# Kernel tuning notes

Hardware: AMD Instinct MI355X
Metric: run time of the kernel (lower is better)

## Reference

```python
import jax, jax.numpy as jnp
import numpy as np

N_EMBEDDING = 32
HEAD_SIZE = 64
B, T = 8, 4096


def setup_inputs() -> dict:
    key = jax.random.key(0)
    kx, kk, kq, kv = jax.random.split(key, 4)
    x = jax.random.normal(kx, (B, T, N_EMBEDDING), dtype=jnp.float32)
    Wk = jax.random.normal(kk, (N_EMBEDDING, HEAD_SIZE), dtype=jnp.float32) * 0.05
    Wq = jax.random.normal(kq, (N_EMBEDDING, HEAD_SIZE), dtype=jnp.float32) * 0.05
    Wv = jax.random.normal(kv, (N_EMBEDDING, HEAD_SIZE), dtype=jnp.float32) * 0.05
    return {"x": x, "Wk": Wk, "Wq": Wq, "Wv": Wv}


def reference(x, Wk, Wq, Wv):
    # x: [B, T, C]; projections (no bias)
    k = jnp.einsum("btc,cd->btd", x, Wk)  # [B,T,D]
    q = jnp.einsum("btc,cd->btd", x, Wq)
    v = jnp.einsum("btc,cd->btd", x, Wv)
    # raw scores (NOTE: original module applies no 1/sqrt(D) scaling)
    wei = jnp.einsum("bqd,bkd->bqk", q, k)  # [B,T,T]
    t = x.shape[1]
    causal = jnp.tril(jnp.ones((t, t), dtype=bool))
    wei = jnp.where(causal[None, :, :], wei, -jnp.inf)
    wei = jax.nn.softmax(wei, axis=-1)
    out = jnp.einsum("bqk,bkd->bqd", wei, v)  # [B,T,D]
    return out
```

## Files before the change

kernel.cpp:

```cpp
#include <hip/hip_runtime.h>
#include <hip/hip_bf16.h>

constexpr int Bc = 8;
constexpr int Tt = 4096;
constexpr int Dd = 64;

typedef __attribute__((ext_vector_type(8))) short short8;
typedef __attribute__((ext_vector_type(4))) float floatx4;
typedef uint4   __attribute__((may_alias)) uint4_a;
typedef short8  __attribute__((may_alias)) short8_a;
typedef ushort4 __attribute__((may_alias)) ushort4_a;
typedef float4  __attribute__((may_alias)) float4_a;

#define MFMA16(A, B, C) __builtin_amdgcn_mfma_f32_16x16x32_bf16(A, B, C, 0, 0, 0)
constexpr float LOG2E = 1.4426950408889634f;

__device__ __forceinline__ unsigned rnd16(float x) {
    unsigned u; __builtin_memcpy(&u, &x, 4); return u + 0x8000u;
}
__device__ __forceinline__ unsigned pk_bf2(float lo, float hi) {
    return __builtin_amdgcn_perm(rnd16(hi), rnd16(lo), 0x07060302);
}
__device__ __forceinline__ ushort4 pack4(floatx4 d) {
    union { unsigned u[2]; ushort4 v; } r;
    r.u[0] = pk_bf2(d[0], d[1]);
    r.u[1] = pk_bf2(d[2], d[3]);
    return r.v;
}
__device__ __forceinline__ short8 cvt8(float4 a, float4 b) {
    union { unsigned u[4]; short8 s; } r;
    r.u[0] = pk_bf2(a.x, a.y);
    r.u[1] = pk_bf2(a.z, a.w);
    r.u[2] = pk_bf2(b.x, b.y);
    r.u[3] = pk_bf2(b.z, b.w);
    return r.s;
}

__global__ __launch_bounds__(1024, 4) void attn_kernel(
    const float* __restrict__ x,
    const float* __restrict__ Wk, const float* __restrict__ Wq,
    const float* __restrict__ Wv,
    float* __restrict__ out)
{
    __shared__ uint4 sStage[4096];
    __shared__ uint4 sP[2048];

    int b  = blockIdx.x & 7;
    int pr = blockIdx.x >> 3;
    int tid  = threadIdx.x;
    int wave = tid >> 6, lane = tid & 63;
    int group = wave >> 2, gw = wave & 3;
    int ln15 = lane & 15, quad = lane >> 4;
    int tid_g = tid & 255;
    size_t bT = (size_t)b * Tt;

    short8 wv_f[4];
    #pragma unroll
    for (int t = 0; t < 4; ++t) {
        int col = 16*t + ln15;
        union { unsigned u[4]; short8 s; } rv;
        #pragma unroll
        for (int jj = 0; jj < 4; ++jj) {
            const float* v0 = Wv + (quad*8 + 2*jj) * 64 + col;
            rv.u[jj] = pk_bf2(v0[0], v0[64]);
        }
        wv_f[t] = rv.s;
    }

    if (wave == 0) {
        floatx4 gC[2][2];
        #pragma unroll
        for (int mt = 0; mt < 2; ++mt)
            #pragma unroll
            for (int nt = 0; nt < 2; ++nt) gC[mt][nt] = (floatx4){0.f,0.f,0.f,0.f};
        #pragma unroll
        for (int kt = 0; kt < 2; ++kt) {
            short8 aG[2], bG[2];
            #pragma unroll
            for (int mt = 0; mt < 2; ++mt) {
                const float* qp = Wq + (ln15 + 16*mt)*64 + 32*kt + quad*8;
                float4 a = ((const float4_a*)qp)[0], bb = ((const float4_a*)qp)[1];
                a.x*=LOG2E; a.y*=LOG2E; a.z*=LOG2E; a.w*=LOG2E;
                bb.x*=LOG2E; bb.y*=LOG2E; bb.z*=LOG2E; bb.w*=LOG2E;
                aG[mt] = cvt8(a, bb);
                const float* kp = Wk + (ln15 + 16*mt)*64 + 32*kt + quad*8;
                bG[mt] = cvt8(((const float4_a*)kp)[0], ((const float4_a*)kp)[1]);
            }
            #pragma unroll
            for (int mt = 0; mt < 2; ++mt)
                #pragma unroll
                for (int nt = 0; nt < 2; ++nt)
                    gC[mt][nt] = MFMA16(aG[mt], bG[nt], gC[mt][nt]);
        }
        unsigned short* sGh = (unsigned short*)sP;
        #pragma unroll
        for (int mt = 0; mt < 2; ++mt)
            #pragma unroll
            for (int nt = 0; nt < 2; ++nt)
                *(ushort4_a*)(sGh + (16*nt + ln15)*32 + 16*mt + quad*4)
                    = pack4(gC[mt][nt]);
    }
    __syncthreads();
    short8 gt[2];
    #pragma unroll
    for (int mt = 0; mt < 2; ++mt) {
        union { uint4 u; short8 s; } g;
        g.u = sP[(16*mt + ln15)*4 + quad];
        gt[mt] = g.s;
    }
    __syncthreads();

    const int gBase = group * 1024;
    const int cT = tid_g & 31, kgT = tid_g >> 5;
    unsigned short* sYh = (unsigned short*)sP;

    #pragma unroll
    for (int phase = 0; phase < 2; ++phase) {
        const int qtP = phase ? pr : 63 - pr;
        const int q0 = qtP * 64;
        const int qrow = q0 + gw*16 + ln15;

        float4 pX0, pX1; float pT[8];
        if (group <= qtP) {
            const float* xp = x + (bT + group*64 + 16*gw + ln15)*32 + quad*8;
            pX0 = ((const float4_a*)xp)[0];
            pX1 = ((const float4_a*)xp)[1];
            const float* tp = x + (bT + group*64 + kgT*8)*32 + cT;
            #pragma unroll
            for (int j = 0; j < 8; ++j) pT[j] = tp[j*32];
        }

        if (wave < 8) {
            int qs = wave & 3, mt = wave >> 2;
            const float* xp = x + (bT + q0 + qs*16 + ln15)*32 + quad*8;
            short8 xq = cvt8(((const float4_a*)xp)[0], ((const float4_a*)xp)[1]);
            floatx4 d = (floatx4){0.f,0.f,0.f,0.f};
            d = MFMA16(gt[mt], xq, d);
            *(ushort4_a*)(sYh + (qs*16 + ln15)*32 + 16*mt + quad*4) = pack4(d);
        }
        __syncthreads();
        short8 bq;
        {
            union { uint4 u; short8 s; } t0;
            t0.u = sP[(gw*16 + ln15)*4 + quad];
            bq = t0.s;
        }

        floatx4 z4[2];
        z4[0] = (floatx4){0.f,0.f,0.f,0.f};
        z4[1] = (floatx4){0.f,0.f,0.f,0.f};
        float l_lane = 0.f;

        const int nIter = (qtP + 4) >> 2;

        for (int it = 0; it < nIter; ++it) {
            int kt = 4*it + group;
            bool active = (kt <= qtP);
            const int stB = gBase + (it & 1) * 512;
            if (active) {
                union { short8 s; uint4 u; } xu;
                xu.s = cvt8(pX0, pX1);
                sStage[stB + (16*gw + ln15)*4 + quad] = xu.u;
                uint4 xt;
                xt.x = pk_bf2(pT[0], pT[1]); xt.y = pk_bf2(pT[2], pT[3]);
                xt.z = pk_bf2(pT[4], pT[5]); xt.w = pk_bf2(pT[6], pT[7]);
                sStage[stB + 256 + cT*8 + (kgT ^ (cT & 7))] = xt;
            }
            __syncthreads();
            int ktn = kt + 4;
            if (ktn <= qtP) {
                const float* xp = x +
                    (bT + ktn*64 + 16*gw + ln15)*32 + quad*8;
                pX0 = ((const float4_a*)xp)[0];
                pX1 = ((const float4_a*)xp)[1];
                const float* tp = x + (bT + ktn*64 + kgT*8)*32 + cT;
                #pragma unroll
                for (int j = 0; j < 8; ++j) pT[j] = tp[j*32];
            }
            if (!active) continue;
            int k0 = kt * 64;

            floatx4 s4[4];
            #pragma unroll
            for (int t = 0; t < 4; ++t) {
                union { uint4 u; short8 s; } a;
                a.u = sStage[stB + (16*t + ln15)*4 + quad];
                floatx4 c = (floatx4){0.f,0.f,0.f,0.f};
                c = MFMA16(a.s, bq, c);
                s4[t] = c;
            }

            unsigned long long* sP64 = (unsigned long long*)sP;
            const int pb = wave*256 + ln15*16;
            const int xk = ln15 & 14;
            if (kt == qtP) {
                #pragma unroll
                for (int t = 0; t < 4; ++t) {
                    int keyb = k0 + 16*t + quad*4;
                    float p[4];
                    #pragma unroll
                    for (int r = 0; r < 4; ++r) {
                        p[r] = (keyb + r <= qrow) ? __builtin_amdgcn_exp2f(s4[t][r]) : 0.f;
                        l_lane += p[r];
                    }
                    unsigned long long pk =
                        ((unsigned long long)pk_bf2(p[2], p[3]) << 32) | pk_bf2(p[0], p[1]);
                    sP64[pb + ((4*t + quad) ^ xk)] = pk;
                }
            } else {
                #pragma unroll
                for (int t = 0; t < 4; ++t) {
                    float p[4];
                    #pragma unroll
                    for (int r = 0; r < 4; ++r) {
                        p[r] = __builtin_amdgcn_exp2f(s4[t][r]);
                        l_lane += p[r];
                    }
                    unsigned long long pk =
                        ((unsigned long long)pk_bf2(p[2], p[3]) << 32) | pk_bf2(p[0], p[1]);
                    sP64[pb + ((4*t + quad) ^ xk)] = pk;
                }
            }

            int h = (ln15 >> 1) & 7;
            union { uint4 u; short8 s; } p0, p1;
            p0.u = sP[wave*128 + ln15*8 + (quad ^ h)];
            p1.u = sP[wave*128 + ln15*8 + ((quad + 4) ^ h)];
            #pragma unroll
            for (int mt = 0; mt < 2; ++mt) {
                int row = 16*mt + ln15;
                union { uint4 u; short8 s; } a0, a1;
                a0.u = sStage[stB + 256 + row*8 + (quad ^ (ln15 & 7))];
                a1.u = sStage[stB + 256 + row*8 + ((4 + quad) ^ (ln15 & 7))];
                z4[mt] = MFMA16(a0.s, p0.s, z4[mt]);
                z4[mt] = MFMA16(a1.s, p1.s, z4[mt]);
            }
        }

        __syncthreads();
        int li = gw*64 + lane;
        ((float*)sP)[wave*64 + lane] = l_lane;
        if (group != 0) {
            float4* st = (float4*)((char*)sStage + group*16384);
            st[li*2 + 0] = make_float4(z4[0][0], z4[0][1], z4[0][2], z4[0][3]);
            st[li*2 + 1] = make_float4(z4[1][0], z4[1][1], z4[1][2], z4[1][3]);
        }
        __syncthreads();
        if (group == 0) {
            float l = l_lane + ((float*)sP)[256 + li]
                    + ((float*)sP)[512 + li] + ((float*)sP)[768 + li];
            l += __shfl_xor(l, 16);
            l += __shfl_xor(l, 32);
            float inv = 1.f / l;
            #pragma unroll
            for (int g = 1; g < 4; ++g) {
                float4* st = (float4*)((char*)sStage + g*16384);
                float4 a = st[li*2 + 0], bb = st[li*2 + 1];
                z4[0][0]+=a.x; z4[0][1]+=a.y; z4[0][2]+=a.z; z4[0][3]+=a.w;
                z4[1][0]+=bb.x; z4[1][1]+=bb.y; z4[1][2]+=bb.z; z4[1][3]+=bb.w;
            }
            unsigned short* sZb = (unsigned short*)sStage;
            #pragma unroll
            for (int mt = 0; mt < 2; ++mt)
                *(ushort4_a*)(sZb + (gw*16 + ln15)*32 + 16*mt + quad*4) = pack4(z4[mt]);
            union { uint4 u; short8 s; } zb;
            zb.u = sStage[(gw*16 + ln15)*4 + quad];
            #pragma unroll
            for (int t = 0; t < 4; ++t) {
                floatx4 o = (floatx4){0.f,0.f,0.f,0.f};
                o = MFMA16(wv_f[t], zb.s, o);
                *(float4_a*)(out + (bT + q0 + gw*16 + ln15)*Dd + 16*t + quad*4)
                    = make_float4(o[0]*inv, o[1]*inv, o[2]*inv, o[3]*inv);
            }
        }
        __syncthreads();
    }
}

extern "C" void kernel_launch(void* const* d_in, const int* in_sizes, int n_in,
                              void* d_out, int out_size, void* d_ws, size_t ws_size,
                              hipStream_t stream)
{
    const float* x  = (const float*)d_in[0];
    const float* Wk = (const float*)d_in[1];
    const float* Wq = (const float*)d_in[2];
    const float* Wv = (const float*)d_in[3];
    float* out = (float*)d_out;

    attn_kernel<<<Bc * 32, 1024, 0, stream>>>(x, Wk, Wq, Wv, out);
}
```

Baseline: 106.3 us.

## Load x once per key tile and build transposed copy in LDS

```diff
diff --git a/kernel.cpp b/kernel.cpp
--- a/kernel.cpp
+++ b/kernel.cpp
@@ -44,6 +44,7 @@
 {
     __shared__ uint4 sStage[4096];
     __shared__ uint4 sP[2048];
+    __shared__ uint4 sG[128];
 
     int b  = blockIdx.x & 7;
     int pr = blockIdx.x >> 3;
@@ -51,21 +52,11 @@
     int wave = tid >> 6, lane = tid & 63;
     int group = wave >> 2, gw = wave & 3;
     int ln15 = lane & 15, quad = lane >> 4;
-    int tid_g = tid & 255;
     size_t bT = (size_t)b * Tt;
 
-    short8 wv_f[4];
-    #pragma unroll
-    for (int t = 0; t < 4; ++t) {
-        int col = 16*t + ln15;
-        union { unsigned u[4]; short8 s; } rv;
-        #pragma unroll
-        for (int jj = 0; jj < 4; ++jj) {
-            const float* v0 = Wv + (quad*8 + 2*jj) * 64 + col;
-            rv.u[jj] = pk_bf2(v0[0], v0[64]);
-        }
-        wv_f[t] = rv.s;
-    }
+    const int tg = tid & 255;
+    const int srow = tg >> 2, scg = tg & 3;
+    const int skg = srow >> 3, srl = srow & 7;
 
     if (wave == 0) {
         floatx4 gC[2][2];
@@ -92,7 +83,7 @@
                 for (int nt = 0; nt < 2; ++nt)
                     gC[mt][nt] = MFMA16(aG[mt], bG[nt], gC[mt][nt]);
         }
-        unsigned short* sGh = (unsigned short*)sP;
+        unsigned short* sGh = (unsigned short*)sG;
         #pragma unroll
         for (int mt = 0; mt < 2; ++mt)
             #pragma unroll
@@ -101,41 +92,30 @@
                     = pack4(gC[mt][nt]);
     }
     __syncthreads();
-    short8 gt[2];
-    #pragma unroll
-    for (int mt = 0; mt < 2; ++mt) {
-        union { uint4 u; short8 s; } g;
-        g.u = sP[(16*mt + ln15)*4 + quad];
-        gt[mt] = g.s;
-    }
-    __syncthreads();
 
     const int gBase = group * 1024;
-    const int cT = tid_g & 31, kgT = tid_g >> 5;
     unsigned short* sYh = (unsigned short*)sP;
 
-    #pragma unroll
     for (int phase = 0; phase < 2; ++phase) {
         const int qtP = phase ? pr : 63 - pr;
         const int q0 = qtP * 64;
         const int qrow = q0 + gw*16 + ln15;
 
-        float4 pX0, pX1; float pT[8];
+        float4 pX0, pX1;
         if (group <= qtP) {
-            const float* xp = x + (bT + group*64 + 16*gw + ln15)*32 + quad*8;
+            const float* xp = x + (bT + group*64 + srow)*32 + scg*8;
             pX0 = ((const float4_a*)xp)[0];
             pX1 = ((const float4_a*)xp)[1];
-            const float* tp = x + (bT + group*64 + kgT*8)*32 + cT;
-            #pragma unroll
-            for (int j = 0; j < 8; ++j) pT[j] = tp[j*32];
         }
 
         if (wave < 8) {
             int qs = wave & 3, mt = wave >> 2;
+            union { uint4 u; short8 s; } g;
+            g.u = sG[(16*mt + ln15)*4 + quad];
             const float* xp = x + (bT + q0 + qs*16 + ln15)*32 + quad*8;
             short8 xq = cvt8(((const float4_a*)xp)[0], ((const float4_a*)xp)[1]);
             floatx4 d = (floatx4){0.f,0.f,0.f,0.f};
-            d = MFMA16(gt[mt], xq, d);
+            d = MFMA16(g.s, xq, d);
             *(ushort4_a*)(sYh + (qs*16 + ln15)*32 + 16*mt + quad*4) = pack4(d);
         }
         __syncthreads();
@@ -158,33 +138,37 @@
             bool active = (kt <= qtP);
             const int stB = gBase + (it & 1) * 512;
             if (active) {
-                union { short8 s; uint4 u; } xu;
-                xu.s = cvt8(pX0, pX1);
-                sStage[stB + (16*gw + ln15)*4 + quad] = xu.u;
-                uint4 xt;
-                xt.x = pk_bf2(pT[0], pT[1]); xt.y = pk_bf2(pT[2], pT[3]);
-                xt.z = pk_bf2(pT[4], pT[5]); xt.w = pk_bf2(pT[6], pT[7]);
-                sStage[stB + 256 + cT*8 + (kgT ^ (cT & 7))] = xt;
+                unsigned u0 = pk_bf2(pX0.x, pX0.y), u1 = pk_bf2(pX0.z, pX0.w);
+                unsigned u2 = pk_bf2(pX1.x, pX1.y), u3 = pk_bf2(pX1.z, pX1.w);
+                uint4 xu; xu.x = u0; xu.y = u1; xu.z = u2; xu.w = u3;
+                sStage[stB + srow*4 + (scg ^ (srow & 3))] = xu;
+                unsigned short* sXh = (unsigned short*)(sStage + stB + 256);
+                int cb = scg * 8;
+                sXh[(cb+0)*64 + ((skg ^ 0) << 3) + srl] = (unsigned short)(u0 & 0xffff);
+                sXh[(cb+1)*64 + ((skg ^ 1) << 3) + srl] = (unsigned short)(u0 >> 16);
+                sXh[(cb+2)*64 + ((skg ^ 2) << 3) + srl] = (unsigned short)(u1 & 0xffff);
+                sXh[(cb+3)*64 + ((skg ^ 3) << 3) + srl] = (unsigned short)(u1 >> 16);
+                sXh[(cb+4)*64 + ((skg ^ 4) << 3) + srl] = (unsigned short)(u2 & 0xffff);
+                sXh[(cb+5)*64 + ((skg ^ 5) << 3) + srl] = (unsigned short)(u2 >> 16);
+                sXh[(cb+6)*64 + ((skg ^ 6) << 3) + srl] = (unsigned short)(u3 & 0xffff);
+                sXh[(cb+7)*64 + ((skg ^ 7) << 3) + srl] = (unsigned short)(u3 >> 16);
             }
             __syncthreads();
             int ktn = kt + 4;
             if (ktn <= qtP) {
-                const float* xp = x +
-                    (bT + ktn*64 + 16*gw + ln15)*32 + quad*8;
+                const float* xp = x + (bT + ktn*64 + srow)*32 + scg*8;
                 pX0 = ((const float4_a*)xp)[0];
                 pX1 = ((const float4_a*)xp)[1];
-                const float* tp = x + (bT + ktn*64 + kgT*8)*32 + cT;
-                #pragma unroll
-                for (int j = 0; j < 8; ++j) pT[j] = tp[j*32];
             }
             if (!active) continue;
             int k0 = kt * 64;
 
+            const int xsw = quad ^ (ln15 & 3);
             floatx4 s4[4];
             #pragma unroll
             for (int t = 0; t < 4; ++t) {
                 union { uint4 u; short8 s; } a;
-                a.u = sStage[stB + (16*t + ln15)*4 + quad];
+                a.u = sStage[stB + (16*t + ln15)*4 + xsw];
                 floatx4 c = (floatx4){0.f,0.f,0.f,0.f};
                 c = MFMA16(a.s, bq, c);
                 s4[t] = c;
@@ -226,12 +210,13 @@
             union { uint4 u; short8 s; } p0, p1;
             p0.u = sP[wave*128 + ln15*8 + (quad ^ h)];
             p1.u = sP[wave*128 + ln15*8 + ((quad + 4) ^ h)];
+            const int h7 = ln15 & 7;
             #pragma unroll
             for (int mt = 0; mt < 2; ++mt) {
                 int row = 16*mt + ln15;
                 union { uint4 u; short8 s; } a0, a1;
-                a0.u = sStage[stB + 256 + row*8 + (quad ^ (ln15 & 7))];
-                a1.u = sStage[stB + 256 + row*8 + ((4 + quad) ^ (ln15 & 7))];
+                a0.u = sStage[stB + 256 + row*8 + (quad ^ h7)];
+                a1.u = sStage[stB + 256 + row*8 + ((quad + 4) ^ h7)];
                 z4[mt] = MFMA16(a0.s, p0.s, z4[mt]);
                 z4[mt] = MFMA16(a1.s, p1.s, z4[mt]);
             }
@@ -241,12 +226,24 @@
         int li = gw*64 + lane;
         ((float*)sP)[wave*64 + lane] = l_lane;
         if (group != 0) {
-            float4* st = (float4*)((char*)sStage + group*16384);
+            float4* st = (float4*)(sStage + group*1024);
             st[li*2 + 0] = make_float4(z4[0][0], z4[0][1], z4[0][2], z4[0][3]);
             st[li*2 + 1] = make_float4(z4[1][0], z4[1][1], z4[1][2], z4[1][3]);
         }
         __syncthreads();
         if (group == 0) {
+            short8 wv_f[4];
+            #pragma unroll
+            for (int t = 0; t < 4; ++t) {
+                int col = 16*t + ln15;
+                union { unsigned u[4]; short8 s; } rv;
+                #pragma unroll
+                for (int jj = 0; jj < 4; ++jj) {
+                    const float* v0 = Wv + (quad*8 + 2*jj) * 64 + col;
+                    rv.u[jj] = pk_bf2(v0[0], v0[64]);
+                }
+                wv_f[t] = rv.s;
+            }
             float l = l_lane + ((float*)sP)[256 + li]
                     + ((float*)sP)[512 + li] + ((float*)sP)[768 + li];
             l += __shfl_xor(l, 16);
@@ -254,7 +251,7 @@
             float inv = 1.f / l;
             #pragma unroll
             for (int g = 1; g < 4; ++g) {
-                float4* st = (float4*)((char*)sStage + g*16384);
+                float4* st = (float4*)(sStage + g*1024);
                 float4 a = st[li*2 + 0], bb = st[li*2 + 1];
                 z4[0][0]+=a.x; z4[0][1]+=a.y; z4[0][2]+=a.z; z4[0][3]+=a.w;
                 z4[1][0]+=bb.x; z4[1][1]+=bb.y; z4[1][2]+=bb.z; z4[1][3]+=bb.w;
```

Result: faster. 90.28 us (-15.1%).
